# Optimization experiments

Hardware: AMD Instinct MI355X
Metric: run time of the kernel (lower is better)

Reference implementation:

```python
import jax, jax.numpy as jnp
import numpy as np

N, F, OUT = 8192, 256, 256


def setup_inputs() -> dict:
    key = jax.random.key(0)
    ks = jax.random.split(key, 8)
    s = 1.0 / np.sqrt(F)
    return {
        "features": jax.random.normal(ks[0], (N, F), jnp.float32),
        "key_features": jax.random.normal(ks[1], (N, F), jnp.float32),
        "adj_matrix": jax.random.uniform(ks[2], (N, N), jnp.float32),
        "W_d": jax.random.normal(ks[3], (2 * F, F), jnp.float32) * (1.0 / np.sqrt(2 * F)),
        "b_d": jnp.zeros((F,), jnp.float32),
        "W_o": jax.random.normal(ks[4], (F, OUT), jnp.float32) * s,
        "b_o": jnp.zeros((OUT,), jnp.float32),
        "W_a": jax.random.normal(ks[5], (F, F), jnp.float32) * s,
        "b_a": jnp.zeros((F,), jnp.float32),
        "W_ao": jax.random.normal(ks[6], (F, OUT), jnp.float32) * s,
        "b_ao": jnp.zeros((OUT,), jnp.float32),
    }


def reference(features, key_features, adj_matrix, W_d, b_d, W_o, b_o, W_a, b_a, W_ao, b_ao):
    n = features.shape[0]
    # masked softmax over rows; self-loop (diagonal) masked out
    neg = jnp.asarray(-1e9, adj_matrix.dtype)
    logits = adj_matrix * 5.0 + jnp.eye(n, dtype=adj_matrix.dtype) * neg
    a = jax.nn.softmax(logits, axis=-1)  # [N, N]
    # sum_j a_ij * concat(x_i, x_j) == concat(x_i * rowsum_i, (A @ X)_i)
    rowsum = jnp.sum(a, axis=-1, keepdims=True)  # == 1, kept for faithfulness
    agg = a @ features  # [N, F]
    neigh = jnp.concatenate([features * rowsum, agg], axis=-1)  # [N, 2F]
    neigh_distill = neigh @ W_d + b_d
    feature_updated = jnp.tanh((features - neigh_distill) @ W_o + b_o)
    # aggregate branch (withAgg=True)
    key_agg = (a @ key_features) @ W_a + b_a
    feature_aggregate = jnp.tanh((key_features + key_agg) @ W_ao + b_ao)
    return (feature_updated, feature_aggregate)
```

## Files before the change

kernel.cpp:

```cpp
#include <hip/hip_runtime.h>
#include <stdint.h>
#include <math.h>


typedef __attribute__((ext_vector_type(4)))  short bf16x4_t;
typedef __attribute__((ext_vector_type(8)))  short bf16x8_t;
typedef __attribute__((ext_vector_type(4)))  float f32x4_t;
typedef __attribute__((ext_vector_type(16))) float f32x16_t;

#define MFMA32(A, B, C) __builtin_amdgcn_mfma_f32_32x32x16_bf16(A, B, C, 0, 0, 0)
#define MFMA16(A, B, C) __builtin_amdgcn_mfma_f32_16x16x32_bf16(A, B, C, 0, 0, 0)

__device__ __forceinline__ unsigned short f2bf(float x) {
    union { float f; unsigned u; } c; c.f = x;
    unsigned u = c.u;
    return (unsigned short)((u + 0x7fffu + ((u >> 16) & 1u)) >> 16);
}
__device__ __forceinline__ unsigned pack2bf(float a, float b) {
    return (unsigned)f2bf(a) | ((unsigned)f2bf(b) << 16);
}
__device__ __forceinline__ float bflo(unsigned u) {
    union { unsigned u; float f; } c; c.u = u << 16; return c.f;
}
__device__ __forceinline__ float bfhi(unsigned u) {
    union { unsigned u; float f; } c; c.u = u & 0xffff0000u; return c.f;
}

__global__ __launch_bounds__(256) void transpose_f32_bf16(
    const float* __restrict__ src, unsigned short* __restrict__ dst, int R, int C)
{
    __shared__ float tile[32][33];
    const int x  = threadIdx.x & 31;
    const int y4 = (threadIdx.x >> 5) * 4;
    const int r0 = blockIdx.x * 32;
    const int c0 = blockIdx.y * 32;
#pragma unroll
    for (int i = 0; i < 4; ++i)
        tile[y4 + i][x] = src[(size_t)(r0 + y4 + i) * C + c0 + x];
    __syncthreads();
#pragma unroll
    for (int i = 0; i < 4; ++i)
        dst[(size_t)(c0 + y4 + i) * R + r0 + x] = f2bf(tile[x][y4 + i]);
}

__global__ __launch_bounds__(256) void pack_half(
    const float* __restrict__ src, unsigned* __restrict__ dst)
{
    const int idx = blockIdx.x * 256 + threadIdx.x;
    const int row = idx >> 7, cp = idx & 127;
    float2 v = *(const float2*)(src + (size_t)row * 256 + cp * 2);
    dst[(size_t)row * 256 + cp] = pack2bf(v.x, v.y);
}

__global__ __launch_bounds__(256) void compose1(
    const float* __restrict__ W_d, const float* __restrict__ W_o,
    unsigned short* __restrict__ W1t)
{
    __shared__ float wrow[256];
    const int k = blockIdx.x, t = threadIdx.x;
    wrow[t] = W_d[(size_t)k * 256 + t];
    __syncthreads();
    float acc = 0.f;
#pragma unroll 8
    for (int m = 0; m < 256; ++m) acc = fmaf(wrow[m], W_o[(size_t)m * 256 + t], acc);
    const float v = (k < 256 ? W_o[(size_t)k * 256 + t] : 0.f) - acc;
    W1t[(size_t)t * 512 + k] = f2bf(v);
}

__global__ __launch_bounds__(256) void compose2(
    const float* __restrict__ W_a, const float* __restrict__ W_ao,
    unsigned short* __restrict__ W2t)
{
    __shared__ float wrow[256];
    const int k = blockIdx.x, t = threadIdx.x;
    float v;
    if (k < 256) {
        v = W_ao[(size_t)k * 256 + t];
    } else {
        wrow[t] = W_a[(size_t)(k - 256) * 256 + t];
        __syncthreads();
        float acc = 0.f;
#pragma unroll 8
        for (int m = 0; m < 256; ++m) acc = fmaf(wrow[m], W_ao[(size_t)m * 256 + t], acc);
        v = acc;
    }
    W2t[(size_t)t * 512 + k] = f2bf(v);
}

__global__ __launch_bounds__(256) void biasC(
    const float* __restrict__ b_d, const float* __restrict__ b_o,
    const float* __restrict__ b_a, const float* __restrict__ b_ao,
    const float* __restrict__ W_o, const float* __restrict__ W_ao,
    float* __restrict__ c1, float* __restrict__ c2)
{
    const int t = threadIdx.x;
    float a1 = 0.f, a2 = 0.f;
#pragma unroll 8
    for (int m = 0; m < 256; ++m) {
        a1 = fmaf(b_d[m], W_o [(size_t)m * 256 + t], a1);
        a2 = fmaf(b_a[m], W_ao[(size_t)m * 256 + t], a2);
    }
    c1[t] = b_o[t] - a1;
    c2[t] = b_ao[t] + a2;
}

#define ROWS 128
#define KSLICE 2048
#define NIT 64
#define NCH 16
#define ASTRIDE 36

__global__ __launch_bounds__(1024) void exp_gemm(
    const float* __restrict__ adj, const unsigned short* __restrict__ Xt,
    unsigned short* __restrict__ Upart, float* __restrict__ sSp)
{
    __shared__ unsigned short sA[2][4][ROWS * ASTRIDE];

    const int t = threadIdx.x;
    const int w = t >> 6, lane = t & 63, q = lane >> 5, l31 = lane & 31;
    const int rb = blockIdx.x >> 2, h = blockIdx.x & 3;
    const int row0 = rb * ROWS, kbase = h * KSLICE;

    const int srow = t >> 3, skoff = (t & 7) * 4;
    const int sgrow = row0 + srow;
    const float* adj_row = adj + (size_t)sgrow * 8192 + kbase + skoff;
    const int swoff = srow * ASTRIDE + skoff;

    const unsigned short* bptr = Xt + (size_t)(w * 32 + l31) * 8192 + kbase + q * 8;

    float rs = 0.f;
    f32x16_t acc[4];
#pragma unroll
    for (int mt = 0; mt < 4; ++mt)
#pragma unroll
        for (int e = 0; e < 16; ++e) acc[mt][e] = 0.f;

    bf16x8_t bq[4][2];
    float4 qaA[4], qaB[4];

    auto stageChunk = [&](int cidx, const float4 (&qa)[4], int buf) {
        unsigned short* sb = &sA[buf][0][0] + swoff;
#pragma unroll
        for (int ks = 0; ks < 4; ++ks) {
            const float4 v = qa[ks];
            float e0 = __expf(5.f * v.x);
            float e1 = __expf(5.f * v.y);
            float e2 = __expf(5.f * v.z);
            float e3 = __expf(5.f * v.w);
            const int gk = kbase + (cidx * 4 + ks) * 32 + skoff;
            if (gk + 0 == sgrow) e0 = 0.f;
            if (gk + 1 == sgrow) e1 = 0.f;
            if (gk + 2 == sgrow) e2 = 0.f;
            if (gk + 3 == sgrow) e3 = 0.f;
            rs += (e0 + e1) + (e2 + e3);
            uint2 p; p.x = pack2bf(e0, e1); p.y = pack2bf(e2, e3);
            *(uint2*)(sb + ks * (ROWS * ASTRIDE)) = p;
        }
    };

    auto phase = [&](int c, float4 (&qaPre)[4], const float4 (&qaStg)[4], int buf) {
        if (c + 2 < NCH) {
#pragma unroll
            for (int ks = 0; ks < 4; ++ks)
                qaPre[ks] = *(const float4*)(adj_row + (size_t)((c + 2) * 4 + ks) * 32);
        }
        if (c + 1 < NCH) stageChunk(c + 1, qaStg, buf ^ 1);
#pragma unroll
        for (int u = 0; u < 4; ++u) {
            const int j = c * 4 + u;
            int jn = j + 2; if (jn >= NIT) jn = 0;
            bq[(u + 2) & 3][0] = *(const bf16x8_t*)(bptr + (size_t)jn * 32);
            bq[(u + 2) & 3][1] = *(const bf16x8_t*)(bptr + (size_t)jn * 32 + 16);
            const unsigned short* sa = &sA[buf][u][0] + l31 * ASTRIDE + q * 8;
#pragma unroll
            for (int s = 0; s < 2; ++s)
#pragma unroll
                for (int mt = 0; mt < 4; ++mt) {
                    const unsigned short* p = sa + mt * (32 * ASTRIDE) + s * 16;
                    bf16x4_t lo = *(const bf16x4_t*)p;
                    bf16x4_t hi = *(const bf16x4_t*)(p + 4);
                    bf16x8_t a = __builtin_shufflevector(lo, hi, 0, 1, 2, 3, 4, 5, 6, 7);
                    acc[mt] = MFMA32(a, bq[u][s], acc[mt]);
                }
        }
        asm volatile("s_waitcnt lgkmcnt(0)\n\ts_barrier" ::: "memory");
    };

#pragma unroll
    for (int ks = 0; ks < 4; ++ks)
        qaA[ks] = *(const float4*)(adj_row + (size_t)ks * 32);
#pragma unroll
    for (int ks = 0; ks < 4; ++ks)
        qaB[ks] = *(const float4*)(adj_row + (size_t)(4 + ks) * 32);
    stageChunk(0, qaA, 0);
    bq[0][0] = *(const bf16x8_t*)(bptr + 0);
    bq[0][1] = *(const bf16x8_t*)(bptr + 16);
    bq[1][0] = *(const bf16x8_t*)(bptr + 32);
    bq[1][1] = *(const bf16x8_t*)(bptr + 48);
    asm volatile("s_waitcnt lgkmcnt(0)\n\ts_barrier" ::: "memory");

    for (int c0 = 0; c0 < NCH; c0 += 2) {
        phase(c0,     qaA, qaB, 0);
        phase(c0 + 1, qaB, qaA, 1);
    }

    rs += __shfl_xor(rs, 1);
    rs += __shfl_xor(rs, 2);
    rs += __shfl_xor(rs, 4);
    if ((t & 7) == 0) sSp[h * 8192 + sgrow] = rs;

    unsigned short* up = Upart + (size_t)h * (8192 * 512) + (size_t)row0 * 512 + (w * 32 + l31);
#pragma unroll
    for (int mt = 0; mt < 4; ++mt)
#pragma unroll
        for (int reg = 0; reg < 16; ++reg) {
            const int lrow = mt * 32 + (reg & 3) + 8 * (reg >> 2) + 4 * q;
            up[(size_t)lrow * 512] = f2bf(acc[mt][reg]);
        }
}

__global__ __launch_bounds__(256) void finalize_agg(
    const unsigned* __restrict__ Upart, const float* __restrict__ sSp,
    unsigned* __restrict__ XcatN, unsigned* __restrict__ Kcat)
{
    const int row = blockIdx.x, t = threadIdx.x;
    const float inv = 1.f / (sSp[row] + sSp[8192 + row] + sSp[16384 + row] + sSp[24576 + row]);
    const unsigned* u = Upart + (size_t)row * 256 + t;
    float lo = 0.f, hi = 0.f;
#pragma unroll
    for (int hh = 0; hh < 4; ++hh) {
        const unsigned v = u[(size_t)hh * (8192 * 256)];
        lo += bflo(v); hi += bfhi(v);
    }
    const unsigned res = pack2bf(lo * inv, hi * inv);
    if (t < 128) XcatN[(size_t)row * 256 + 128 + t] = res;
    else         Kcat [(size_t)row * 256 + t];
    if (t >= 128) Kcat[(size_t)row * 256 + t] = res;
}

__global__ __launch_bounds__(256) void gemm_out(
    const unsigned short* __restrict__ A, const unsigned short* __restrict__ Wt,
    const float* __restrict__ cvec, float* __restrict__ out)
{
    __shared__ unsigned short sAm[32 * ASTRIDE];
    __shared__ unsigned short sB[256 * ASTRIDE];
    __shared__ float sBias[256];

    const int t = threadIdx.x, w = t >> 6, lane = t & 63;
    const int m_lo = lane & 15, quad = lane >> 4;
    const int row0 = blockIdx.x * 32;
    sBias[t] = cvec[t];

    f32x4_t acc[2][4];
#pragma unroll
    for (int a = 0; a < 2; ++a)
#pragma unroll
        for (int b = 0; b < 4; ++b)
#pragma unroll
            for (int e = 0; e < 4; ++e) acc[a][b][e] = 0.f;

    for (int ks = 0; ks < 16; ++ks) {
        const int k0 = ks * 32;
        __syncthreads();
        if (t < 128) {
            bf16x8_t v = *(const bf16x8_t*)(A + (size_t)(row0 + (t >> 2)) * 512 + k0 + (t & 3) * 8);
            unsigned short* d = &sAm[(t >> 2) * ASTRIDE + (t & 3) * 8];
            *(bf16x4_t*)d       = __builtin_shufflevector(v, v, 0, 1, 2, 3);
            *(bf16x4_t*)(d + 4) = __builtin_shufflevector(v, v, 4, 5, 6, 7);
        }
        {
            const unsigned short* src = Wt + (size_t)t * 512 + k0;
            unsigned short* d = &sB[t * ASTRIDE];
#pragma unroll
            for (int j = 0; j < 4; ++j) {
                bf16x8_t v = *(const bf16x8_t*)(src + j * 8);
                *(bf16x4_t*)(d + j * 8)     = __builtin_shufflevector(v, v, 0, 1, 2, 3);
                *(bf16x4_t*)(d + j * 8 + 4) = __builtin_shufflevector(v, v, 4, 5, 6, 7);
            }
        }
        __syncthreads();
        bf16x8_t a0, a1;
        {
            const unsigned short* p = &sAm[m_lo * ASTRIDE + quad * 8];
            bf16x4_t lo = *(const bf16x4_t*)p, hi = *(const bf16x4_t*)(p + 4);
            a0 = __builtin_shufflevector(lo, hi, 0, 1, 2, 3, 4, 5, 6, 7);
            p += 16 * ASTRIDE;
            lo = *(const bf16x4_t*)p; hi = *(const bf16x4_t*)(p + 4);
            a1 = __builtin_shufflevector(lo, hi, 0, 1, 2, 3, 4, 5, 6, 7);
        }
#pragma unroll
        for (int nt = 0; nt < 4; ++nt) {
            const unsigned short* p = &sB[(w * 64 + nt * 16 + m_lo) * ASTRIDE + quad * 8];
            bf16x4_t lo = *(const bf16x4_t*)p, hi = *(const bf16x4_t*)(p + 4);
            bf16x8_t b = __builtin_shufflevector(lo, hi, 0, 1, 2, 3, 4, 5, 6, 7);
            acc[0][nt] = MFMA16(a0, b, acc[0][nt]);
            acc[1][nt] = MFMA16(a1, b, acc[1][nt]);
        }
    }

#pragma unroll
    for (int mt = 0; mt < 2; ++mt)
#pragma unroll
        for (int nt = 0; nt < 4; ++nt) {
            const int col = w * 64 + nt * 16 + m_lo;
#pragma unroll
            for (int r = 0; r < 4; ++r) {
                const int row = row0 + mt * 16 + quad * 4 + r;
                out[(size_t)row * 256 + col] = tanhf(acc[mt][nt][r] + sBias[col]);
            }
        }
}

extern "C" void kernel_launch(void* const* d_in, const int* in_sizes, int n_in,
                              void* d_out, int out_size, void* d_ws, size_t ws_size,
                              hipStream_t stream) {
    const float* features = (const float*)d_in[0];
    const float* key      = (const float*)d_in[1];
    const float* adj      = (const float*)d_in[2];
    const float* W_d  = (const float*)d_in[3];
    const float* b_d  = (const float*)d_in[4];
    const float* W_o  = (const float*)d_in[5];
    const float* b_o  = (const float*)d_in[6];
    const float* W_a  = (const float*)d_in[7];
    const float* b_a  = (const float*)d_in[8];
    const float* W_ao = (const float*)d_in[9];
    const float* b_ao = (const float*)d_in[10];

    float* out1 = (float*)d_out;
    float* out2 = out1 + (size_t)8192 * 256;

    char* ws = (char*)d_ws;
    unsigned short* XcatN = (unsigned short*)(ws);
    unsigned short* Kcat  = (unsigned short*)(ws +  8388608);
    unsigned short* Xt    = (unsigned short*)(ws + 16777216);
    unsigned short* Upart = (unsigned short*)(ws + 25165824);
    float*          sSp   = (float*)         (ws + 58720256);
    unsigned short* W1t   = (unsigned short*)(ws + 58851328);
    unsigned short* W2t   = (unsigned short*)(ws + 59113472);
    float*          c1    = (float*)         (ws + 59375616);
    float*          c2    = (float*)         (ws + 59376640);

    dim3 blk(256);
    transpose_f32_bf16<<<dim3(256, 8), blk, 0, stream>>>(features, Xt, 8192, 256);
    transpose_f32_bf16<<<dim3(256, 8), blk, 0, stream>>>(key, Xt + (size_t)256 * 8192, 8192, 256);
    pack_half<<<4096, blk, 0, stream>>>(features, (unsigned*)XcatN);
    pack_half<<<4096, blk, 0, stream>>>(key, (unsigned*)Kcat);
    compose1<<<512, blk, 0, stream>>>(W_d, W_o, W1t);
    compose2<<<512, blk, 0, stream>>>(W_a, W_ao, W2t);
    biasC<<<1, blk, 0, stream>>>(b_d, b_o, b_a, b_ao, W_o, W_ao, c1, c2);

    exp_gemm<<<256, dim3(1024), 0, stream>>>(adj, Xt, Upart, sSp);
    finalize_agg<<<8192, blk, 0, stream>>>((const unsigned*)Upart, sSp,
                                           (unsigned*)XcatN, (unsigned*)Kcat);

    gemm_out<<<256, blk, 0, stream>>>(XcatN, W1t, c1, out1);
    gemm_out<<<256, blk, 0, stream>>>(Kcat,  W2t, c2, out2);
}
```

Measured before the change: 603.9 us.

## Store partial accumulators in fragment-native layout and merge output GEMM launches

exp_gemm now writes its partial results as packed bf16 pairs in the MFMA fragment order, so each store is a contiguous per-lane word instead of a strided 2-byte scatter. finalize_agg reads these blocks with vector loads, transposes them through shared memory and writes coalesced 16-byte outputs. The two output GEMMs are merged into one launch over 16-row tiles, which cuts launch overhead and doubles the block count, at the cost of reloading the weight tile once per 16 rows instead of once per 32.

```diff
diff --git a/kernel.cpp b/kernel.cpp
--- a/kernel.cpp
+++ b/kernel.cpp
@@ -112,7 +112,7 @@
 
 __global__ __launch_bounds__(1024) void exp_gemm(
     const float* __restrict__ adj, const unsigned short* __restrict__ Xt,
-    unsigned short* __restrict__ Upart, float* __restrict__ sSp)
+    unsigned* __restrict__ UpartB, float* __restrict__ sSp)
 {
     __shared__ unsigned short sA[2][4][ROWS * ASTRIDE];
 
@@ -209,60 +209,107 @@
     rs += __shfl_xor(rs, 4);
     if ((t & 7) == 0) sSp[h * 8192 + sgrow] = rs;
 
-    unsigned short* up = Upart + (size_t)h * (8192 * 512) + (size_t)row0 * 512 + (w * 32 + l31);
+    unsigned* up = UpartB + (((size_t)h * 64 + rb) * 16 + w) * 2048 + lane;
 #pragma unroll
     for (int mt = 0; mt < 4; ++mt)
 #pragma unroll
-        for (int reg = 0; reg < 16; ++reg) {
-            const int lrow = mt * 32 + (reg & 3) + 8 * (reg >> 2) + 4 * q;
-            up[(size_t)lrow * 512] = f2bf(acc[mt][reg]);
-        }
+        for (int ip = 0; ip < 8; ++ip)
+            up[(size_t)(mt * 8 + ip) * 64] = pack2bf(acc[mt][2 * ip], acc[mt][2 * ip + 1]);
 }
 
 __global__ __launch_bounds__(256) void finalize_agg(
-    const unsigned* __restrict__ Upart, const float* __restrict__ sSp,
+    const unsigned* __restrict__ UpartB, const float* __restrict__ sSp,
     unsigned* __restrict__ XcatN, unsigned* __restrict__ Kcat)
 {
-    const int row = blockIdx.x, t = threadIdx.x;
-    const float inv = 1.f / (sSp[row] + sSp[8192 + row] + sSp[16384 + row] + sSp[24576 + row]);
-    const unsigned* u = Upart + (size_t)row * 256 + t;
-    float lo = 0.f, hi = 0.f;
-#pragma unroll
-    for (int hh = 0; hh < 4; ++hh) {
-        const unsigned v = u[(size_t)hh * (8192 * 256)];
-        lo += bflo(v); hi += bfhi(v);
-    }
-    const unsigned res = pack2bf(lo * inv, hi * inv);
-    if (t < 128) XcatN[(size_t)row * 256 + 128 + t] = res;
-    else         Kcat [(size_t)row * 256 + t];
-    if (t >= 128) Kcat[(size_t)row * 256 + t] = res;
+    __shared__ float sT[128][65];
+    __shared__ float sInv[128];
+
+    const int t = threadIdx.x;
+    const int rb = blockIdx.x >> 3, wp = blockIdx.x & 7;
+    const int row0 = rb * 128;
+
+    if (t < 128) {
+        const int r = row0 + t;
+        sInv[t] = 1.f / (sSp[r] + sSp[8192 + r] + sSp[16384 + r] + sSp[24576 + r]);
+    }
+
+    const int i = t >> 3;
+    const int l0 = (t & 7) * 8;
+    const int mt = i >> 3, ip = i & 7;
+    const int qq = l0 >> 5;
+    const int rlo = mt * 32 + 2 * (ip & 1) + 8 * (ip >> 1) + 4 * qq;
+    const int cbase = l0 & 31;
+
+#pragma unroll
+    for (int wi = 0; wi < 2; ++wi) {
+        const int wv = wp * 2 + wi;
+        float lo[8], hi[8];
+#pragma unroll
+        for (int j = 0; j < 8; ++j) { lo[j] = 0.f; hi[j] = 0.f; }
+#pragma unroll
+        for (int h = 0; h < 4; ++h) {
+            const unsigned* src = UpartB + (((size_t)h * 64 + rb) * 16 + wv) * 2048
+                                  + (size_t)i * 64 + l0;
+            const uint4 v0 = *(const uint4*)(src);
+            const uint4 v1 = *(const uint4*)(src + 4);
+            const unsigned vv[8] = { v0.x, v0.y, v0.z, v0.w, v1.x, v1.y, v1.z, v1.w };
+#pragma unroll
+            for (int j = 0; j < 8; ++j) { lo[j] += bflo(vv[j]); hi[j] += bfhi(vv[j]); }
+        }
+#pragma unroll
+        for (int j = 0; j < 8; ++j) {
+            sT[rlo][wi * 32 + cbase + j]     = lo[j];
+            sT[rlo + 1][wi * 32 + cbase + j] = hi[j];
+        }
+    }
+    __syncthreads();
+
+    const int row = t >> 1, cg = (t & 1) * 32;
+    const float inv = sInv[row];
+    unsigned outv[16];
+#pragma unroll
+    for (int j = 0; j < 16; ++j)
+        outv[j] = pack2bf(sT[row][cg + 2 * j] * inv, sT[row][cg + 2 * j + 1] * inv);
+    unsigned* dst = (wp < 4 ? XcatN : Kcat)
+                    + (size_t)(row0 + row) * 256 + 128 + (wp & 3) * 32 + (cg >> 1);
+#pragma unroll
+    for (int j = 0; j < 4; ++j)
+        *(uint4*)(dst + 4 * j) = *(const uint4*)(outv + 4 * j);
 }
 
 __global__ __launch_bounds__(256) void gemm_out(
-    const unsigned short* __restrict__ A, const unsigned short* __restrict__ Wt,
-    const float* __restrict__ cvec, float* __restrict__ out)
-{
-    __shared__ unsigned short sAm[32 * ASTRIDE];
+    const unsigned short* __restrict__ Aa, const unsigned short* __restrict__ Wta,
+    const float* __restrict__ ca,
+    const unsigned short* __restrict__ Ab, const unsigned short* __restrict__ Wtb,
+    const float* __restrict__ cb,
+    float* __restrict__ outa, float* __restrict__ outb)
+{
+    __shared__ unsigned short sAm[16 * ASTRIDE];
     __shared__ unsigned short sB[256 * ASTRIDE];
     __shared__ float sBias[256];
 
+    const int bid = blockIdx.x;
+    const int prob = bid >> 9, tile = bid & 511;
+    const unsigned short* A  = prob ? Ab  : Aa;
+    const unsigned short* Wt = prob ? Wtb : Wta;
+    const float* cvec        = prob ? cb  : ca;
+    float* out               = prob ? outb : outa;
+
     const int t = threadIdx.x, w = t >> 6, lane = t & 63;
     const int m_lo = lane & 15, quad = lane >> 4;
-    const int row0 = blockIdx.x * 32;
+    const int row0 = tile * 16;
     sBias[t] = cvec[t];
 
-    f32x4_t acc[2][4];
-#pragma unroll
-    for (int a = 0; a < 2; ++a)
-#pragma unroll
-        for (int b = 0; b < 4; ++b)
-#pragma unroll
-            for (int e = 0; e < 4; ++e) acc[a][b][e] = 0.f;
+    f32x4_t acc[4];
+#pragma unroll
+    for (int b = 0; b < 4; ++b)
+#pragma unroll
+        for (int e = 0; e < 4; ++e) acc[b][e] = 0.f;
 
     for (int ks = 0; ks < 16; ++ks) {
         const int k0 = ks * 32;
         __syncthreads();
-        if (t < 128) {
+        if (t < 64) {
             bf16x8_t v = *(const bf16x8_t*)(A + (size_t)(row0 + (t >> 2)) * 512 + k0 + (t & 3) * 8);
             unsigned short* d = &sAm[(t >> 2) * ASTRIDE + (t & 3) * 8];
             *(bf16x4_t*)d       = __builtin_shufflevector(v, v, 0, 1, 2, 3);
@@ -279,36 +326,30 @@
             }
         }
         __syncthreads();
-        bf16x8_t a0, a1;
+        bf16x8_t a0;
         {
             const unsigned short* p = &sAm[m_lo * ASTRIDE + quad * 8];
             bf16x4_t lo = *(const bf16x4_t*)p, hi = *(const bf16x4_t*)(p + 4);
             a0 = __builtin_shufflevector(lo, hi, 0, 1, 2, 3, 4, 5, 6, 7);
-            p += 16 * ASTRIDE;
-            lo = *(const bf16x4_t*)p; hi = *(const bf16x4_t*)(p + 4);
-            a1 = __builtin_shufflevector(lo, hi, 0, 1, 2, 3, 4, 5, 6, 7);
         }
 #pragma unroll
         for (int nt = 0; nt < 4; ++nt) {
             const unsigned short* p = &sB[(w * 64 + nt * 16 + m_lo) * ASTRIDE + quad * 8];
             bf16x4_t lo = *(const bf16x4_t*)p, hi = *(const bf16x4_t*)(p + 4);
             bf16x8_t b = __builtin_shufflevector(lo, hi, 0, 1, 2, 3, 4, 5, 6, 7);
-            acc[0][nt] = MFMA16(a0, b, acc[0][nt]);
-            acc[1][nt] = MFMA16(a1, b, acc[1][nt]);
-        }
-    }
-
-#pragma unroll
-    for (int mt = 0; mt < 2; ++mt)
-#pragma unroll
-        for (int nt = 0; nt < 4; ++nt) {
-            const int col = w * 64 + nt * 16 + m_lo;
-#pragma unroll
-            for (int r = 0; r < 4; ++r) {
-                const int row = row0 + mt * 16 + quad * 4 + r;
-                out[(size_t)row * 256 + col] = tanhf(acc[mt][nt][r] + sBias[col]);
-            }
-        }
+            acc[nt] = MFMA16(a0, b, acc[nt]);
+        }
+    }
+
+#pragma unroll
+    for (int nt = 0; nt < 4; ++nt) {
+        const int col = w * 64 + nt * 16 + m_lo;
+#pragma unroll
+        for (int r = 0; r < 4; ++r) {
+            const int row = row0 + quad * 4 + r;
+            out[(size_t)row * 256 + col] = tanhf(acc[nt][r] + sBias[col]);
+        }
+    }
 }
 
 extern "C" void kernel_launch(void* const* d_in, const int* in_sizes, int n_in,
@@ -333,7 +374,7 @@
     unsigned short* XcatN = (unsigned short*)(ws);
     unsigned short* Kcat  = (unsigned short*)(ws +  8388608);
     unsigned short* Xt    = (unsigned short*)(ws + 16777216);
-    unsigned short* Upart = (unsigned short*)(ws + 25165824);
+    unsigned*       UpartB= (unsigned*)      (ws + 25165824);
     float*          sSp   = (float*)         (ws + 58720256);
     unsigned short* W1t   = (unsigned short*)(ws + 58851328);
     unsigned short* W2t   = (unsigned short*)(ws + 59113472);
@@ -349,10 +390,9 @@
     compose2<<<512, blk, 0, stream>>>(W_a, W_ao, W2t);
     biasC<<<1, blk, 0, stream>>>(b_d, b_o, b_a, b_ao, W_o, W_ao, c1, c2);
 
-    exp_gemm<<<256, dim3(1024), 0, stream>>>(adj, Xt, Upart, sSp);
-    finalize_agg<<<8192, blk, 0, stream>>>((const unsigned*)Upart, sSp,
-                                           (unsigned*)XcatN, (unsigned*)Kcat);
-
-    gemm_out<<<256, blk, 0, stream>>>(XcatN, W1t, c1, out1);
-    gemm_out<<<256, blk, 0, stream>>>(Kcat,  W2t, c2, out2);
-}
+    exp_gemm<<<256, dim3(1024), 0, stream>>>(adj, Xt, UpartB, sSp);
+    finalize_agg<<<512, blk, 0, stream>>>(UpartB, sSp,
+                                          (unsigned*)XcatN, (unsigned*)Kcat);
+
+    gemm_out<<<1024, blk, 0, stream>>>(XcatN, W1t, c1, Kcat, W2t, c2, out1, out2);
+}
```

Result: no change. 596.9 us (-1.2%).
